# Kernel tuning notes

Hardware: AMD Instinct MI355X
Metric: run time of the kernel (lower is better)

Reference implementation:

```python
import jax, jax.numpy as jnp
import numpy as np

NEG_SLOPE = 0.2


def gat_conv(x, src, dst, N, W, a_src, a_dst, b, concat):
    # x: [N, F_in], W: [F_in, H*C], a_src/a_dst: [H, C], b: [H*C] or [C]
    H, C = a_src.shape
    h = (x @ W).reshape(N, H, C)                    # [N, H, C]
    al_src = jnp.einsum('nhc,hc->nh', h, a_src)     # [N, H]
    al_dst = jnp.einsum('nhc,hc->nh', h, a_dst)     # [N, H]
    logits = jax.nn.leaky_relu(al_src[src] + al_dst[dst], NEG_SLOPE)  # [E, H]
    # edge softmax over incoming edges of each destination node
    m = jax.ops.segment_max(logits, dst, num_segments=N)              # [N, H]
    m = jnp.where(jnp.isfinite(m), m, 0.0)
    e = jnp.exp(logits - m[dst])                                      # [E, H]
    denom = jax.ops.segment_sum(e, dst, num_segments=N)               # [N, H]
    alpha = e / denom[dst]                                            # [E, H]
    out = jax.ops.segment_sum(alpha[:, :, None] * h[src], dst, num_segments=N)  # [N, H, C]
    if concat:
        return out.reshape(N, H * C) + b
    return out.mean(axis=1) + b


def setup_inputs() -> dict:
    key = jax.random.key(0)
    ks = jax.random.split(key, 12)
    N, E = 100000, 1600000
    F_in, Ch, Co, H = 128, 32, 64, 4
    x = jax.random.normal(ks[0], (N, F_in), dtype=jnp.float32)
    edge_index = jax.random.randint(ks[1], (2, E), 0, N, dtype=jnp.int64)
    s = 0.1
    return {
        'x': x, 'edge_index': edge_index,
        'W1': jax.random.normal(ks[2], (F_in, H * Ch), jnp.float32) * s,
        'a_src1': jax.random.normal(ks[3], (H, Ch), jnp.float32) * s,
        'a_dst1': jax.random.normal(ks[4], (H, Ch), jnp.float32) * s,
        'b1': jnp.zeros((H * Ch,), jnp.float32),
        'W2': jax.random.normal(ks[5], (H * Ch, H * Ch), jnp.float32) * s,
        'a_src2': jax.random.normal(ks[6], (H, Ch), jnp.float32) * s,
        'a_dst2': jax.random.normal(ks[7], (H, Ch), jnp.float32) * s,
        'b2': jnp.zeros((H * Ch,), jnp.float32),
        'W3': jax.random.normal(ks[8], (H * Ch, H * Co), jnp.float32) * s,
        'a_src3': jax.random.normal(ks[9], (H, Co), jnp.float32) * s,
        'a_dst3': jax.random.normal(ks[10], (H, Co), jnp.float32) * s,
        'b3': jnp.zeros((Co,), jnp.float32),
    }


def reference(x, edge_index, W1, a_src1, a_dst1, b1, W2, a_src2, a_dst2, b2, W3, a_src3, a_dst3, b3):
    N = x.shape[0]
    # PyG GATConv default add_self_loops=True
    loop = jnp.arange(N, dtype=edge_index.dtype)
    src = jnp.concatenate([edge_index[0], loop])
    dst = jnp.concatenate([edge_index[1], loop])
    h = gat_conv(x, src, dst, N, W1, a_src1, a_dst1, b1, concat=True)
    h = jax.nn.elu(h)
    h = gat_conv(h, src, dst, N, W2, a_src2, a_dst2, b2, concat=True)
    h = jax.nn.elu(h)
    out = gat_conv(h, src, dst, N, W3, a_src3, a_dst3, b3, concat=False)
    return out
```

## Files before the change

kernel.cpp:

```cpp
#include <hip/hip_runtime.h>


#define NEG_SLOPE 0.2f

typedef __attribute__((ext_vector_type(8))) _Float16 half8v;
typedef __attribute__((ext_vector_type(2))) _Float16 half2v;
typedef __attribute__((ext_vector_type(4))) float f32x4;

__device__ __forceinline__ float lrelu(float v) { return v > 0.f ? v : NEG_SLOPE * v; }

struct hf2 { _Float16 hi, lo; };
__device__ __forceinline__ hf2 split_f16(float f)
{
    hf2 r;
    r.hi = (_Float16)f;
    r.lo = (_Float16)(f - (float)r.hi);
    return r;
}

__global__ void fill_sentinel(float* __restrict__ out, int n)
{
    int i = blockIdx.x * blockDim.x + threadIdx.x;
    if (i < n) out[i] = 1e30f;
}

__global__ void detect_idx64(const int* __restrict__ ei, int* __restrict__ flag)
{
    __shared__ int anynz;
    if (threadIdx.x == 0) anynz = 0;
    __syncthreads();
    int v = ei[2 * threadIdx.x + 1];
    if (v != 0) atomicOr(&anynz, 1);
    __syncthreads();
    if (threadIdx.x == 0) flag[0] = (anynz == 0) ? 1 : 0;
}

__global__ void convert_edges(const void* __restrict__ ei, const int* __restrict__ flag,
                              int* __restrict__ src32, int* __restrict__ dst32, int E)
{
    int e = blockIdx.x * blockDim.x + threadIdx.x;
    if (e >= E) return;
    if (flag[0]) {
        src32[e] = (int)((const long long*)ei)[e];
        dst32[e] = (int)((const long long*)ei)[E + e];
    } else {
        src32[e] = ((const int*)ei)[e];
        dst32[e] = ((const int*)ei)[E + e];
    }
}

__global__ void count_deg(const int* __restrict__ dst32, int* __restrict__ deg,
                          int* __restrict__ loc, int E)
{
    int e = blockIdx.x * blockDim.x + threadIdx.x;
    if (e >= E) return;
    loc[e] = atomicAdd(&deg[dst32[e]], 1);
}

__global__ __launch_bounds__(256)
void scanA(const int* __restrict__ deg, int* __restrict__ rowptr,
           int* __restrict__ bsum, int N)
{
    __shared__ int part[256];
    const int t = threadIdx.x;
    const int base = blockIdx.x * 1024 + t * 4;
    int v[4];
    #pragma unroll
    for (int j = 0; j < 4; ++j) v[j] = (base + j < N) ? deg[base + j] : 0;
    int s = v[0] + v[1] + v[2] + v[3];
    part[t] = s;
    __syncthreads();
    #pragma unroll
    for (int off = 1; off < 256; off <<= 1) {
        int p = (t >= off) ? part[t - off] : 0;
        __syncthreads();
        part[t] += p;
        __syncthreads();
    }
    int run = (t == 0) ? 0 : part[t - 1];
    #pragma unroll
    for (int j = 0; j < 4; ++j) {
        if (base + j < N) rowptr[base + j] = run;
        run += v[j];
    }
    if (t == 255) bsum[blockIdx.x] = part[255];
}

__global__ __launch_bounds__(1024)
void scanB(int* __restrict__ bsum, int nb)
{
    __shared__ int s[1024];
    int t = threadIdx.x;
    s[t] = (t < nb) ? bsum[t] : 0;
    __syncthreads();
    for (int off = 1; off < 1024; off <<= 1) {
        int p = (t >= off) ? s[t - off] : 0;
        __syncthreads();
        s[t] += p;
        __syncthreads();
    }
    if (t < nb) bsum[t] = (t == 0) ? 0 : s[t - 1];
}

__global__ __launch_bounds__(256)
void scanC(int* __restrict__ rowptr, const int* __restrict__ bsum, int N, int E)
{
    const int base = blockIdx.x * 1024 + threadIdx.x * 4;
    const int off = bsum[blockIdx.x];
    #pragma unroll
    for (int j = 0; j < 4; ++j)
        if (base + j < N) rowptr[base + j] += off;
    if (blockIdx.x == 0 && threadIdx.x == 0) rowptr[N] = E;
}

__global__ void fill_csr(const int* __restrict__ src32, const int* __restrict__ dst32,
                         const int* __restrict__ loc, const int* __restrict__ rowptr,
                         int* __restrict__ csr_src, int E)
{
    int e = blockIdx.x * blockDim.x + threadIdx.x;
    if (e >= E) return;
    csr_src[rowptr[dst32[e]] + loc[e]] = src32[e];
}

__global__ void convert_hilo(const float* __restrict__ in, _Float16* __restrict__ hi,
                             _Float16* __restrict__ lo, long long n4)
{
    long long t = (long long)blockIdx.x * blockDim.x + threadIdx.x;
    if (t >= n4) return;
    float4 v = *(const float4*)&in[t * 4];
    hf2 a = split_f16(v.x), b = split_f16(v.y), c = split_f16(v.z), d = split_f16(v.w);
    __attribute__((ext_vector_type(4))) _Float16 h, l;
    h.x = a.hi; h.y = b.hi; h.z = c.hi; h.w = d.hi;
    l.x = a.lo; l.y = b.lo; l.z = c.lo; l.w = d.lo;
    *(decltype(h)*)&hi[t * 4] = h;
    *(decltype(l)*)&lo[t * 4] = l;
}

__global__ __launch_bounds__(256)
void convert_wt(const float* __restrict__ W, _Float16* __restrict__ wthi,
                _Float16* __restrict__ wtlo, int ldw, int wcol0)
{
    int t = blockIdx.x * 256 + threadIdx.x;
    int k = t >> 7, n = t & 127;
    float v = W[(long long)k * ldw + wcol0 + n];
    hf2 r = split_f16(v);
    wthi[n * 128 + k] = r.hi;
    wtlo[n * 128 + k] = r.lo;
}

template<int HPC>
__global__ __launch_bounds__(256)
void gemm_mfma(const _Float16* __restrict__ Ahi, const _Float16* __restrict__ Alo,
               const _Float16* __restrict__ Wthi, const _Float16* __restrict__ Wtlo,
               _Float16* __restrict__ Chi,
               const float* __restrict__ aS, const float* __restrict__ aD,
               float* __restrict__ als, float* __restrict__ ald, int M)
{
    const int tid = threadIdx.x;
    const int wave = tid >> 6, lane = tid & 63;
    const int l15 = lane & 15, lk = lane >> 4;
    const int m0 = blockIdx.x * 64 + wave * 16;
    int mrow = m0 + l15;
    if (mrow >= M) mrow = M - 1;

    f32x4 acc[8];
    #pragma unroll
    for (int i = 0; i < 8; ++i) acc[i] = (f32x4){0.f, 0.f, 0.f, 0.f};

    #pragma unroll
    for (int kt = 0; kt < 4; ++kt) {
        const int k = kt * 32 + lk * 8;
        half8v ah = *(const half8v*)&Ahi[(long long)mrow * 128 + k];
        half8v al = *(const half8v*)&Alo[(long long)mrow * 128 + k];
        #pragma unroll
        for (int nf = 0; nf < 8; ++nf) {
            half8v bh = *(const half8v*)&Wthi[(nf * 16 + l15) * 128 + k];
            half8v bl = *(const half8v*)&Wtlo[(nf * 16 + l15) * 128 + k];
            acc[nf] = __builtin_amdgcn_mfma_f32_16x16x32_f16(ah, bh, acc[nf], 0, 0, 0);
            acc[nf] = __builtin_amdgcn_mfma_f32_16x16x32_f16(ah, bl, acc[nf], 0, 0, 0);
            acc[nf] = __builtin_amdgcn_mfma_f32_16x16x32_f16(al, bh, acc[nf], 0, 0, 0);
        }
    }

    #pragma unroll
    for (int r = 0; r < 4; ++r) {
        int gm = m0 + lk * 4 + r;
        if (gm >= M) continue;
        #pragma unroll
        for (int nf = 0; nf < 8; ++nf)
            Chi[(long long)gm * 128 + nf * 16 + l15] = (_Float16)acc[nf][r];
    }

    float asv[8], adv[8];
    #pragma unroll
    for (int nf = 0; nf < 8; ++nf) {
        asv[nf] = aS[nf * 16 + l15];
        adv[nf] = aD[nf * 16 + l15];
    }
    constexpr int NFH = 8 / HPC;
    #pragma unroll
    for (int r = 0; r < 4; ++r) {
        #pragma unroll
        for (int h = 0; h < HPC; ++h) {
            float ps = 0.f, pd = 0.f;
            #pragma unroll
            for (int q = 0; q < NFH; ++q) {
                int nf = h * NFH + q;
                ps += acc[nf][r] * asv[nf];
                pd += acc[nf][r] * adv[nf];
            }
            #pragma unroll
            for (int m = 1; m < 16; m <<= 1) {
                ps += __shfl_xor(ps, m);
                pd += __shfl_xor(pd, m);
            }
            if (l15 == 0) {
                int gm = m0 + lk * 4 + r;
                if (gm < M) {
                    als[gm * HPC + h] = ps;
                    ald[gm * HPC + h] = pd;
                }
            }
        }
    }
}

template<int C, int HL, bool MEAN, bool ACCUM>
__global__ __launch_bounds__(256)
void gat_aggregate(const int* __restrict__ rowptr, const int* __restrict__ csr_src,
                   const float* __restrict__ als, const float* __restrict__ ald,
                   const _Float16* __restrict__ h16, const float* __restrict__ bias,
                   float* __restrict__ out,
                   _Float16* __restrict__ ohi, _Float16* __restrict__ olo, int N)
{
    constexpr int ROW = HL * C;
    constexpr int LOG2HL = (HL == 4) ? 2 : 1;
    const int d = (blockIdx.x * blockDim.x + threadIdx.x) >> 6;
    const int lane = threadIdx.x & 63;
    if (d >= N) return;
    const int j = lane * 2;
    const int hh = j / C;

    const int myh = lane & (HL - 1);
    const int myi = lane >> LOG2HL;
    const float ald_mine = ald[d * HL + myh];

    const float ald_d = (HL == 4 && myh == hh) ? ald_mine : ald[d * HL + hh];
    const float wself = __expf(lrelu(als[d * HL + hh] + ald_d));
    float denom = wself;
    half2v hv = *(const half2v*)&h16[(unsigned)d * ROW + j];
    float vx = wself * (float)hv.x, vy = wself * (float)hv.y;

    const int e0 = rowptr[d], e1 = rowptr[d + 1];
    for (int base = e0; base < e1; base += 8) {
        int ee = base + myi;
        int sv_mine = csr_src[ee < e1 ? ee : e1 - 1];
        float a = als[sv_mine * HL + myh] + ald_mine;
        float w_mine = (ee < e1) ? __expf(lrelu(a)) : 0.f;

        int sref[8];
        half2v hb[8];
        #pragma unroll
        for (int i = 0; i < 8; ++i) sref[i] = __shfl(sv_mine, i * HL, 64);
        #pragma unroll
        for (int i = 0; i < 8; ++i) hb[i] = *(const half2v*)&h16[(unsigned)sref[i] * ROW + j];
        #pragma unroll
        for (int i = 0; i < 8; ++i) {
            float wv = __shfl(w_mine, i * HL + hh, 64);
            denom += wv;
            vx += wv * (float)hb[i].x;
            vy += wv * (float)hb[i].y;
        }
    }
    float inv = 1.f / denom;
    vx *= inv; vy *= inv;

    if (!MEAN) {
        vx += bias[j]; vy += bias[j + 1];
        vx = vx > 0.f ? vx : __expf(vx) - 1.f;
        vy = vy > 0.f ? vy : __expf(vy) - 1.f;
        hf2 rx = split_f16(vx), ry = split_f16(vy);
        half2v hi2, lo2;
        hi2.x = rx.hi; hi2.y = ry.hi;
        lo2.x = rx.lo; lo2.y = ry.lo;
        *(half2v*)&ohi[(unsigned)d * ROW + j] = hi2;
        *(half2v*)&olo[(unsigned)d * ROW + j] = lo2;
    } else {
        vx = 0.25f * vx + __shfl_xor(0.25f * vx, 32);
        vy = 0.25f * vy + __shfl_xor(0.25f * vy, 32);
        if (lane < 32) {
            float* op = &out[(unsigned)d * C + j];
            if (ACCUM) { vx += op[0] + bias[j]; vy += op[1] + bias[j + 1]; }
            *(float2*)op = make_float2(vx, vy);
        }
    }
}

extern "C" void kernel_launch(void* const* d_in, const int* in_sizes, int n_in,
                              void* d_out, int out_size, void* d_ws, size_t ws_size,
                              hipStream_t stream)
{
    const float* x      = (const float*)d_in[0];
    const void*  ei     = d_in[1];
    const float* W1     = (const float*)d_in[2];
    const float* a_src1 = (const float*)d_in[3];
    const float* a_dst1 = (const float*)d_in[4];
    const float* b1     = (const float*)d_in[5];
    const float* W2     = (const float*)d_in[6];
    const float* a_src2 = (const float*)d_in[7];
    const float* a_dst2 = (const float*)d_in[8];
    const float* b2     = (const float*)d_in[9];
    const float* W3     = (const float*)d_in[10];
    const float* a_src3 = (const float*)d_in[11];
    const float* a_dst3 = (const float*)d_in[12];
    const float* b3     = (const float*)d_in[13];

    const int N = in_sizes[0] / 128;
    const int E = in_sizes[1] / 2;

    char* w = (char*)d_ws;
    auto alloc = [&](size_t bytes) {
        char* p = w;
        w += (bytes + 255) & ~(size_t)255;
        return p;
    };
    int*      flag    = (int*)     alloc(256);
    int*      deg     = (int*)     alloc((size_t)N * 4);
    int*      rowptr  = (int*)     alloc((size_t)(N + 1) * 4);
    int*      bsum    = (int*)     alloc(1024 * 4);
    int*      src32   = (int*)     alloc((size_t)E * 4);
    int*      dst32   = (int*)     alloc((size_t)E * 4);
    int*      loc     = (int*)     alloc((size_t)E * 4);
    int*      csr_src = (int*)     alloc((size_t)E * 4);
    _Float16* hhi     = (_Float16*)alloc((size_t)N * 128 * 2);
    _Float16* xhi     = (_Float16*)alloc((size_t)N * 128 * 2);
    _Float16* xlo     = (_Float16*)alloc((size_t)N * 128 * 2);
    float*    als     = (float*)   alloc((size_t)N * 4 * 4);
    float*    ald     = (float*)   alloc((size_t)N * 4 * 4);
    _Float16* wthi    = (_Float16*)alloc(128 * 128 * 2);
    _Float16* wtlo    = (_Float16*)alloc(128 * 128 * 2);
    if ((size_t)(w - (char*)d_ws) > ws_size) {
        fill_sentinel<<<(out_size + 255) / 256, 256, 0, stream>>>((float*)d_out, out_size);
        return;
    }

    const int gb = 256;
    const int nb1024 = (N + 1023) / 1024;
    const int mb = (N + 63) / 64;
    const int ab = (N * 64 + gb - 1) / gb;
    auto blocks = [&](long long tot) { return (int)((tot + gb - 1) / gb); };

    detect_idx64<<<1, 256, 0, stream>>>((const int*)ei, flag);
    convert_edges<<<blocks(E), gb, 0, stream>>>(ei, flag, src32, dst32, E);
    (void)hipMemsetAsync(deg, 0, (size_t)N * 4, stream);
    count_deg<<<blocks(E), gb, 0, stream>>>(dst32, deg, loc, E);
    scanA<<<nb1024, gb, 0, stream>>>(deg, rowptr, bsum, N);
    scanB<<<1, 1024, 0, stream>>>(bsum, nb1024);
    scanC<<<nb1024, gb, 0, stream>>>(rowptr, bsum, N, E);
    fill_csr<<<blocks(E), gb, 0, stream>>>(src32, dst32, loc, rowptr, csr_src, E);

    convert_hilo<<<blocks((long long)N * 32), gb, 0, stream>>>(x, xhi, xlo, (long long)N * 32);

    convert_wt<<<64, gb, 0, stream>>>(W1, wthi, wtlo, 128, 0);
    gemm_mfma<4><<<mb, gb, 0, stream>>>(xhi, xlo, wthi, wtlo, hhi,
                                        a_src1, a_dst1, als, ald, N);
    gat_aggregate<32, 4, false, false><<<ab, gb, 0, stream>>>(
        rowptr, csr_src, als, ald, hhi, b1, nullptr, xhi, xlo, N);

    convert_wt<<<64, gb, 0, stream>>>(W2, wthi, wtlo, 128, 0);
    gemm_mfma<4><<<mb, gb, 0, stream>>>(xhi, xlo, wthi, wtlo, hhi,
                                        a_src2, a_dst2, als, ald, N);
    gat_aggregate<32, 4, false, false><<<ab, gb, 0, stream>>>(
        rowptr, csr_src, als, ald, hhi, b2, nullptr, xhi, xlo, N);

    convert_wt<<<64, gb, 0, stream>>>(W3, wthi, wtlo, 256, 0);
    gemm_mfma<2><<<mb, gb, 0, stream>>>(xhi, xlo, wthi, wtlo, hhi,
                                        a_src3, a_dst3, als, ald, N);
    gat_aggregate<64, 2, true, false><<<ab, gb, 0, stream>>>(
        rowptr, csr_src, als, ald, hhi, b3, (float*)d_out, nullptr, nullptr, N);

    convert_wt<<<64, gb, 0, stream>>>(W3, wthi, wtlo, 256, 128);
    gemm_mfma<2><<<mb, gb, 0, stream>>>(xhi, xlo, wthi, wtlo, hhi,
                                        a_src3 + 128, a_dst3 + 128, als, ald, N);
    gat_aggregate<64, 2, true, true><<<ab, gb, 0, stream>>>(
        rowptr, csr_src, als, ald, hhi, b3, (float*)d_out, nullptr, nullptr, N);
}
```

Before: 694.8 us.

## Split aggregate wavefront into two edge halves with 8-byte feature loads

The aggregation kernel now has each half-wavefront handle alternate edges, with every lane loading four fp16 features (8 bytes) instead of two. The two halves are combined with a cross-half shuffle reduction before normalisation. Edge conversion and degree counting are merged into one kernel, which saves a launch and a re-read of dst32. The intent is wider gather loads and fewer serial loop iterations per edge batch, at the cost of extra shuffles and an idle upper half during the epilogue.

```diff
diff --git a/kernel.cpp b/kernel.cpp
--- a/kernel.cpp
+++ b/kernel.cpp
@@ -4,7 +4,7 @@
 #define NEG_SLOPE 0.2f
 
 typedef __attribute__((ext_vector_type(8))) _Float16 half8v;
-typedef __attribute__((ext_vector_type(2))) _Float16 half2v;
+typedef __attribute__((ext_vector_type(4))) _Float16 half4v;
 typedef __attribute__((ext_vector_type(4))) float f32x4;
 
 __device__ __forceinline__ float lrelu(float v) { return v > 0.f ? v : NEG_SLOPE * v; }
@@ -35,26 +35,18 @@
     if (threadIdx.x == 0) flag[0] = (anynz == 0) ? 1 : 0;
 }
 
-__global__ void convert_edges(const void* __restrict__ ei, const int* __restrict__ flag,
-                              int* __restrict__ src32, int* __restrict__ dst32, int E)
+__global__ void prep_edges(const void* __restrict__ ei, const int* __restrict__ flag,
+                           int* __restrict__ src32, int* __restrict__ dst32,
+                           int* __restrict__ deg, int* __restrict__ loc, int E)
 {
     int e = blockIdx.x * blockDim.x + threadIdx.x;
     if (e >= E) return;
-    if (flag[0]) {
-        src32[e] = (int)((const long long*)ei)[e];
-        dst32[e] = (int)((const long long*)ei)[E + e];
-    } else {
-        src32[e] = ((const int*)ei)[e];
-        dst32[e] = ((const int*)ei)[E + e];
-    }
-}
-
-__global__ void count_deg(const int* __restrict__ dst32, int* __restrict__ deg,
-                          int* __restrict__ loc, int E)
-{
-    int e = blockIdx.x * blockDim.x + threadIdx.x;
-    if (e >= E) return;
-    loc[e] = atomicAdd(&deg[dst32[e]], 1);
+    int s, d;
+    if (flag[0]) { s = (int)((const long long*)ei)[e]; d = (int)((const long long*)ei)[E + e]; }
+    else         { s = ((const int*)ei)[e];            d = ((const int*)ei)[E + e]; }
+    src32[e] = s;
+    dst32[e] = d;
+    loc[e] = atomicAdd(&deg[d], 1);
 }
 
 __global__ __launch_bounds__(256)
@@ -129,11 +121,11 @@
     if (t >= n4) return;
     float4 v = *(const float4*)&in[t * 4];
     hf2 a = split_f16(v.x), b = split_f16(v.y), c = split_f16(v.z), d = split_f16(v.w);
-    __attribute__((ext_vector_type(4))) _Float16 h, l;
+    half4v h, l;
     h.x = a.hi; h.y = b.hi; h.z = c.hi; h.w = d.hi;
     l.x = a.lo; l.y = b.lo; l.z = c.lo; l.w = d.lo;
-    *(decltype(h)*)&hi[t * 4] = h;
-    *(decltype(l)*)&lo[t * 4] = l;
+    *(half4v*)&hi[t * 4] = h;
+    *(half4v*)&lo[t * 4] = l;
 }
 
 __global__ __launch_bounds__(256)
@@ -238,60 +230,88 @@
     const int d = (blockIdx.x * blockDim.x + threadIdx.x) >> 6;
     const int lane = threadIdx.x & 63;
     if (d >= N) return;
-    const int j = lane * 2;
-    const int hh = j / C;
+    const int sub = lane & 31;
+    const int half = lane >> 5;
+    const int q = sub * 4;
+    const int chd = q / C;
 
     const int myh = lane & (HL - 1);
     const int myi = lane >> LOG2HL;
     const float ald_mine = ald[d * HL + myh];
 
-    const float ald_d = (HL == 4 && myh == hh) ? ald_mine : ald[d * HL + hh];
-    const float wself = __expf(lrelu(als[d * HL + hh] + ald_d));
-    float denom = wself;
-    half2v hv = *(const half2v*)&h16[(unsigned)d * ROW + j];
-    float vx = wself * (float)hv.x, vy = wself * (float)hv.y;
+    float vx0 = 0.f, vx1 = 0.f, vx2 = 0.f, vx3 = 0.f, dn = 0.f;
+    if (half == 0) {
+        const float wself = __expf(lrelu(als[d * HL + chd] + ald[d * HL + chd]));
+        half4v hs = *(const half4v*)&h16[(unsigned)d * ROW + q];
+        dn = wself;
+        vx0 = wself * (float)hs.x; vx1 = wself * (float)hs.y;
+        vx2 = wself * (float)hs.z; vx3 = wself * (float)hs.w;
+    }
 
     const int e0 = rowptr[d], e1 = rowptr[d + 1];
     for (int base = e0; base < e1; base += 8) {
-        int ee = base + myi;
-        int sv_mine = csr_src[ee < e1 ? ee : e1 - 1];
-        float a = als[sv_mine * HL + myh] + ald_mine;
-        float w_mine = (ee < e1) ? __expf(lrelu(a)) : 0.f;
-
-        int sref[8];
-        half2v hb[8];
-        #pragma unroll
-        for (int i = 0; i < 8; ++i) sref[i] = __shfl(sv_mine, i * HL, 64);
-        #pragma unroll
-        for (int i = 0; i < 8; ++i) hb[i] = *(const half2v*)&h16[(unsigned)sref[i] * ROW + j];
-        #pragma unroll
-        for (int i = 0; i < 8; ++i) {
-            float wv = __shfl(w_mine, i * HL + hh, 64);
-            denom += wv;
-            vx += wv * (float)hb[i].x;
-            vy += wv * (float)hb[i].y;
-        }
-    }
-    float inv = 1.f / denom;
-    vx *= inv; vy *= inv;
-
+        int sv_mine = 0;
+        float w_mine = 0.f;
+        if (lane < 8 * HL) {
+            int ee = base + myi;
+            sv_mine = csr_src[ee < e1 ? ee : e1 - 1];
+            float a = als[sv_mine * HL + myh] + ald_mine;
+            w_mine = (ee < e1) ? __expf(lrelu(a)) : 0.f;
+        }
+        int srefs[4];
+        #pragma unroll
+        for (int r = 0; r < 4; ++r)
+            srefs[r] = __shfl(sv_mine, (2 * r + half) * HL, 64);
+        half4v hb[4];
+        #pragma unroll
+        for (int r = 0; r < 4; ++r)
+            hb[r] = *(const half4v*)&h16[(unsigned)srefs[r] * ROW + q];
+        #pragma unroll
+        for (int r = 0; r < 4; ++r) {
+            float wv = __shfl(w_mine, (2 * r + half) * HL + chd, 64);
+            dn += wv;
+            vx0 += wv * (float)hb[r].x;
+            vx1 += wv * (float)hb[r].y;
+            vx2 += wv * (float)hb[r].z;
+            vx3 += wv * (float)hb[r].w;
+        }
+    }
+    vx0 += __shfl_xor(vx0, 32); vx1 += __shfl_xor(vx1, 32);
+    vx2 += __shfl_xor(vx2, 32); vx3 += __shfl_xor(vx3, 32);
+    dn  += __shfl_xor(dn, 32);
+    if (half != 0) return;
+
+    const float inv = 1.f / dn;
     if (!MEAN) {
-        vx += bias[j]; vy += bias[j + 1];
-        vx = vx > 0.f ? vx : __expf(vx) - 1.f;
-        vy = vy > 0.f ? vy : __expf(vy) - 1.f;
-        hf2 rx = split_f16(vx), ry = split_f16(vy);
-        half2v hi2, lo2;
-        hi2.x = rx.hi; hi2.y = ry.hi;
-        lo2.x = rx.lo; lo2.y = ry.lo;
-        *(half2v*)&ohi[(unsigned)d * ROW + j] = hi2;
-        *(half2v*)&olo[(unsigned)d * ROW + j] = lo2;
+        float o[4] = {vx0 * inv, vx1 * inv, vx2 * inv, vx3 * inv};
+        half4v hi4, lo4;
+        #pragma unroll
+        for (int k = 0; k < 4; ++k) {
+            float v = o[k] + bias[q + k];
+            v = v > 0.f ? v : __expf(v) - 1.f;
+            hf2 s = split_f16(v);
+            if (k == 0) { hi4.x = s.hi; lo4.x = s.lo; }
+            else if (k == 1) { hi4.y = s.hi; lo4.y = s.lo; }
+            else if (k == 2) { hi4.z = s.hi; lo4.z = s.lo; }
+            else { hi4.w = s.hi; lo4.w = s.lo; }
+        }
+        *(half4v*)&ohi[(unsigned)d * ROW + q] = hi4;
+        *(half4v*)&olo[(unsigned)d * ROW + q] = lo4;
     } else {
-        vx = 0.25f * vx + __shfl_xor(0.25f * vx, 32);
-        vy = 0.25f * vy + __shfl_xor(0.25f * vy, 32);
-        if (lane < 32) {
-            float* op = &out[(unsigned)d * C + j];
-            if (ACCUM) { vx += op[0] + bias[j]; vy += op[1] + bias[j + 1]; }
-            *(float2*)op = make_float2(vx, vy);
+        float m0 = 0.25f * vx0 * inv, m1 = 0.25f * vx1 * inv;
+        float m2 = 0.25f * vx2 * inv, m3 = 0.25f * vx3 * inv;
+        m0 += __shfl_xor(m0, 16); m1 += __shfl_xor(m1, 16);
+        m2 += __shfl_xor(m2, 16); m3 += __shfl_xor(m3, 16);
+        if (sub < 16) {
+            float* op = &out[(unsigned)d * C + q];
+            if (ACCUM) {
+                float4 prev = *(const float4*)op;
+                m0 += prev.x + bias[q + 0];
+                m1 += prev.y + bias[q + 1];
+                m2 += prev.z + bias[q + 2];
+                m3 += prev.w + bias[q + 3];
+            }
+            *(float4*)op = make_float4(m0, m1, m2, m3);
         }
     }
 }
@@ -351,9 +371,8 @@
     auto blocks = [&](long long tot) { return (int)((tot + gb - 1) / gb); };
 
     detect_idx64<<<1, 256, 0, stream>>>((const int*)ei, flag);
-    convert_edges<<<blocks(E), gb, 0, stream>>>(ei, flag, src32, dst32, E);
     (void)hipMemsetAsync(deg, 0, (size_t)N * 4, stream);
-    count_deg<<<blocks(E), gb, 0, stream>>>(dst32, deg, loc, E);
+    prep_edges<<<blocks(E), gb, 0, stream>>>(ei, flag, src32, dst32, deg, loc, E);
     scanA<<<nb1024, gb, 0, stream>>>(deg, rowptr, bsum, N);
     scanB<<<1, 1024, 0, stream>>>(bsum, nb1024);
     scanC<<<nb1024, gb, 0, stream>>>(rowptr, bsum, N, E);
```

Measured after the change: 705.9 us. Within noise of the previous version (+1.6%).
